# Performance work log

Measured on AMD Instinct MI355X. Metric: run time of the kernel, lower is better.

## Reference

```python
import jax, jax.numpy as jnp
import numpy as np

TOPK_POS = 16
TOPK_NEG = 16
EPS = 1e-12  # F.normalize default eps


def _l2norm(x):
    # torch.nn.functional.normalize(p=2, dim=1): x / max(||x||_2, eps)
    n = jnp.sqrt(jnp.sum(x * x, axis=1, keepdims=True))
    return x / jnp.maximum(n, EPS)


def setup_inputs() -> dict:
    key = jax.random.key(0)
    k0, k1, k2, k3, k4 = jax.random.split(key, 5)
    B, I, J, C = 32, 1024, 2048, 1024
    f_rad = jax.random.normal(k0, (B, I), dtype=jnp.float32)
    f_histo = jax.random.normal(k1, (B, J), dtype=jnp.float32)
    rad_mask = jax.random.randint(k2, (B,), 0, 2).astype(bool)
    histo_mask = jax.random.randint(k3, (B,), 0, 2).astype(bool)
    # nn.Linear(in_channels*2, out_channels): weight [C, 2*I], bias [C]
    W = jax.random.normal(k4, (C, 2 * I), dtype=jnp.float32) / np.sqrt(2 * I)
    b = jnp.zeros((C,), dtype=jnp.float32)
    token = jnp.zeros((1, C), dtype=jnp.float32)  # missing_modality_token
    return {"f_rad": f_rad, "f_histo": f_histo, "rad_mask": rad_mask,
            "histo_mask": histo_mask, "W": W, "b": b, "token": token}


def reference(f_rad, f_histo, rad_mask, histo_mask, W, b, token):
    r = _l2norm(f_rad)            # [B, I]
    h = _l2norm(f_histo)          # [B, J]
    sim = jnp.einsum('bi,bj->bij', r, h)  # [B, I, J]
    pos_map = jnp.mean(jax.lax.top_k(sim, TOPK_POS)[0], axis=-1)    # [B, I]
    neg_map = jnp.mean(jax.lax.top_k(-sim, TOPK_NEG)[0], axis=-1)   # [B, I]
    # cat([B,1,I],[B,1,I], dim=1).view(B,-1) == concat(pos, neg) along features
    feat = jnp.concatenate([pos_map, neg_map], axis=1)  # [B, 2I]
    emb = feat @ W.T + b                                 # [B, C]
    # modality_flags = ~torch.min(rad_mask, histo_mask)  (bool AND then NOT)
    flags = (~(rad_mask & histo_mask)).astype(emb.dtype)[:, None]  # [B, 1]
    return emb + token * flags
```

## Files before the change

kernel.cpp:

```cpp
#include <hip/hip_runtime.h>
#include <math.h>

#define NB 32
#define NI 1024
#define NJ 2048
#define NC 1024
#define K2 2048

__device__ __forceinline__ void merge16(float* __restrict__ v,
                                        const float* __restrict__ w) {
    float m[16];
#pragma unroll
    for (int i = 0; i < 16; ++i) m[i] = fmaxf(v[i], w[15 - i]);
#pragma unroll
    for (int st = 8; st >= 1; st >>= 1)
#pragma unroll
        for (int i = 0; i < 16; ++i)
            if ((i & st) == 0) {
                float x = m[i], y = m[i + st];
                m[i] = fmaxf(x, y);
                m[i + st] = fminf(x, y);
            }
#pragma unroll
    for (int i = 0; i < 16; ++i) v[i] = m[i];
}

__global__ __launch_bounds__(256)
void prep_kernel(const float* __restrict__ f_rad,
                 const float* __restrict__ f_histo,
                 const unsigned char* __restrict__ rad_mask,
                 const unsigned char* __restrict__ histo_mask,
                 const float* __restrict__ bias,
                 const float* __restrict__ token,
                 float* __restrict__ F,
                 float* __restrict__ out)
{
    __shared__ float listsP[256][16];
    __shared__ float listsN[256][16];
    __shared__ float red[4];

    const int b = blockIdx.x;
    const int t = threadIdx.x;
    const int wave = t >> 6, lane = t & 63;

    float hv[8];
    float ss = 0.f;
#pragma unroll
    for (int i = 0; i < 8; ++i) {
        hv[i] = f_histo[b * NJ + t + i * 256];
        ss += hv[i] * hv[i];
    }
#pragma unroll
    for (int off = 1; off < 64; off <<= 1) ss += __shfl_xor(ss, off, 64);
    if (lane == 0) red[wave] = ss;

    float vp[16], vn[16];
#pragma unroll
    for (int i = 0; i < 8; ++i) { vp[i] = hv[i]; vn[i] = -hv[i]; }
#pragma unroll
    for (int i = 8; i < 16; ++i) { vp[i] = -INFINITY; vn[i] = -INFINITY; }
#pragma unroll
    for (int a = 0; a < 7; ++a)
#pragma unroll
        for (int c = 0; c < 7 - a; ++c) {
            float x = vp[c], y = vp[c + 1];
            vp[c] = fmaxf(x, y); vp[c + 1] = fminf(x, y);
            x = vn[c]; y = vn[c + 1];
            vn[c] = fmaxf(x, y); vn[c + 1] = fminf(x, y);
        }

    __syncthreads();
    const float hnorm = fmaxf(sqrtf(red[0] + red[1] + red[2] + red[3]), 1e-12f);

#pragma unroll
    for (int i = 0; i < 16; ++i) { listsP[t][i] = vp[i]; listsN[t][i] = vn[i]; }
    __syncthreads();

#pragma unroll
    for (int s = 128; s >= 1; s >>= 1) {
        if (t < s) {
            float wp[16], wn[16];
#pragma unroll
            for (int i = 0; i < 16; ++i) { wp[i] = listsP[t + s][i]; wn[i] = listsN[t + s][i]; }
            merge16(vp, wp);
            merge16(vn, wn);
#pragma unroll
            for (int i = 0; i < 16; ++i) { listsP[t][i] = vp[i]; listsN[t][i] = vn[i]; }
        }
        __syncthreads();
    }

    float sumP = 0.f, sumN = 0.f;
#pragma unroll
    for (int i = 0; i < 16; ++i) { sumP += listsP[0][i]; sumN += listsN[0][i]; }
    const float Hpos = sumP / (16.f * hnorm);
    const float Hneg = -sumN / (16.f * hnorm);

    float rv[4];
    float ss2 = 0.f;
#pragma unroll
    for (int i = 0; i < 4; ++i) {
        rv[i] = f_rad[b * NI + t + i * 256];
        ss2 += rv[i] * rv[i];
    }
#pragma unroll
    for (int off = 1; off < 64; off <<= 1) ss2 += __shfl_xor(ss2, off, 64);
    __syncthreads();
    if (lane == 0) red[wave] = ss2;
    __syncthreads();
    const float rnorm = fmaxf(sqrtf(red[0] + red[1] + red[2] + red[3]), 1e-12f);

#pragma unroll
    for (int i = 0; i < 4; ++i) {
        float rn = rv[i] / rnorm;
        float p, q;
        if (rn > 0.f) { p = rn * Hpos;  q = -rn * Hneg; }
        else          { p = rn * Hneg;  q = -rn * Hpos; }
        F[b * K2 + t + i * 256]      = p;
        F[b * K2 + NI + t + i * 256] = q;
    }

    const float flag = (rad_mask[b] != 0 && histo_mask[b] != 0) ? 0.f : 1.f;
#pragma unroll
    for (int i = 0; i < NC / 256; ++i) {
        int c = t + i * 256;
        out[b * NC + c] = bias[c] + token[c] * flag;
    }
}

__global__ __launch_bounds__(256, 4)
void gemm_kernel(const float4* __restrict__ F4,
                 const float4* __restrict__ WF4,
                 float* __restrict__ out)
{
    const int t = threadIdx.x;
    const int wave = t >> 6, lane = t & 63;
    const int c0 = blockIdx.x * 8 + wave * 2;
    const int kk4 = blockIdx.y * 64 + lane;

    const float4 w0 = WF4[(size_t)c0 * 512 + kk4];
    const float4 w1 = WF4[(size_t)(c0 + 1) * 512 + kk4];

    float acc0[32], acc1[32];
#pragma unroll
    for (int b = 0; b < 32; ++b) { acc0[b] = 0.f; acc1[b] = 0.f; }

#pragma unroll
    for (int bb = 0; bb < 32; bb += 4) {
        float4 fv[4];
#pragma unroll
        for (int u = 0; u < 4; ++u) fv[u] = F4[(bb + u) * 512 + kk4];
#pragma unroll
        for (int u = 0; u < 4; ++u) {
            const int b = bb + u;
            acc0[b] = fmaf(fv[u].x, w0.x, acc0[b]);
            acc0[b] = fmaf(fv[u].y, w0.y, acc0[b]);
            acc0[b] = fmaf(fv[u].z, w0.z, acc0[b]);
            acc0[b] = fmaf(fv[u].w, w0.w, acc0[b]);
            acc1[b] = fmaf(fv[u].x, w1.x, acc1[b]);
            acc1[b] = fmaf(fv[u].y, w1.y, acc1[b]);
            acc1[b] = fmaf(fv[u].z, w1.z, acc1[b]);
            acc1[b] = fmaf(fv[u].w, w1.w, acc1[b]);
        }
    }

    const bool odd = lane & 1;
    float z[32];
#pragma unroll
    for (int b = 0; b < 32; ++b) {
        float send = odd ? acc0[b] : acc1[b];
        float recv = __shfl_xor(send, 1, 64);
        z[b] = (odd ? acc1[b] : acc0[b]) + recv;
    }

#pragma unroll
    for (int j = 0; j < 5; ++j) {
        const int o = 2 << j;
        const bool hi = (lane & o) != 0;
        const int n = 32 >> (j + 1);
#pragma unroll
        for (int m = 0; m < n; ++m) {
            float send = hi ? z[2 * m] : z[2 * m + 1];
            float recv = __shfl_xor(send, o, 64);
            z[m] = (hi ? z[2 * m + 1] : z[2 * m]) + recv;
        }
    }

    atomicAdd(&out[(lane >> 1) * NC + c0 + (lane & 1)], z[0]);
}

extern "C" void kernel_launch(void* const* d_in, const int* in_sizes, int n_in,
                              void* d_out, int out_size, void* d_ws, size_t ws_size,
                              hipStream_t stream) {
    const float* f_rad       = (const float*)d_in[0];
    const float* f_histo     = (const float*)d_in[1];
    const unsigned char* rm  = (const unsigned char*)d_in[2];
    const unsigned char* hm  = (const unsigned char*)d_in[3];
    const float* W           = (const float*)d_in[4];
    const float* bias        = (const float*)d_in[5];
    const float* token       = (const float*)d_in[6];
    float* out = (float*)d_out;
    float* F   = (float*)d_ws;

    prep_kernel<<<NB, 256, 0, stream>>>(f_rad, f_histo, rm, hm, bias, token, F, out);
    dim3 grid(128, 8);
    gemm_kernel<<<grid, 256, 0, stream>>>((const float4*)F, (const float4*)W, out);
}
```

Before: 90.74 us.

## Replace shared-memory top-k tree reduction with wave shuffle merges and vectorize prep loads

The prep kernel's 8-level shared-memory tree reduction of per-thread top-16 lists, which needed a block barrier at every level, is replaced by intra-wave shuffle-based bitonic merges, followed by a small final merge of four per-wave lists in shared memory. All global loads and stores in prep (histo, rad, bias, token, F, out) become float4 accesses, and the rad norm reduction is computed alongside the histo norm to drop extra barriers. The aim is to cut the serialized reduction latency of the 32-block prep kernel. In exchange it does many register shuffles, and every thread redundantly performs the final 4-way merge.

```diff
diff --git a/kernel.cpp b/kernel.cpp
--- a/kernel.cpp
+++ b/kernel.cpp
@@ -25,107 +25,149 @@
     for (int i = 0; i < 16; ++i) v[i] = m[i];
 }
 
+__device__ __forceinline__ void merge8to16(const float* __restrict__ a,
+                                           const float* __restrict__ w,
+                                           float* __restrict__ m) {
+#pragma unroll
+    for (int i = 0; i < 8; ++i) m[i] = a[i];
+#pragma unroll
+    for (int i = 0; i < 8; ++i) m[8 + i] = w[7 - i];
+#pragma unroll
+    for (int st = 8; st >= 1; st >>= 1)
+#pragma unroll
+        for (int i = 0; i < 16; ++i)
+            if ((i & st) == 0) {
+                float x = m[i], y = m[i + st];
+                m[i] = fmaxf(x, y);
+                m[i + st] = fminf(x, y);
+            }
+}
+
+__device__ __forceinline__ void sort8_desc(float* __restrict__ v) {
+#pragma unroll
+    for (int a = 0; a < 7; ++a)
+#pragma unroll
+        for (int c = 0; c < 7 - a; ++c) {
+            float x = v[c], y = v[c + 1];
+            v[c] = fmaxf(x, y);
+            v[c + 1] = fminf(x, y);
+        }
+}
+
 __global__ __launch_bounds__(256)
-void prep_kernel(const float* __restrict__ f_rad,
-                 const float* __restrict__ f_histo,
+void prep_kernel(const float4* __restrict__ R4,
+                 const float4* __restrict__ H4,
                  const unsigned char* __restrict__ rad_mask,
                  const unsigned char* __restrict__ histo_mask,
-                 const float* __restrict__ bias,
-                 const float* __restrict__ token,
-                 float* __restrict__ F,
-                 float* __restrict__ out)
+                 const float4* __restrict__ bias4,
+                 const float4* __restrict__ token4,
+                 float4* __restrict__ F4,
+                 float4* __restrict__ out4)
 {
-    __shared__ float listsP[256][16];
-    __shared__ float listsN[256][16];
-    __shared__ float red[4];
+    __shared__ __align__(16) float wlP[4][16];
+    __shared__ __align__(16) float wlN[4][16];
+    __shared__ float redH[4], redR[4];
 
     const int b = blockIdx.x;
     const int t = threadIdx.x;
     const int wave = t >> 6, lane = t & 63;
 
-    float hv[8];
-    float ss = 0.f;
-#pragma unroll
-    for (int i = 0; i < 8; ++i) {
-        hv[i] = f_histo[b * NJ + t + i * 256];
-        ss += hv[i] * hv[i];
-    }
+    const float4 h0 = H4[b * 512 + t];
+    const float4 h1 = H4[b * 512 + 256 + t];
+    const float4 rv4 = R4[b * 256 + t];
+    const float4 bv = bias4[t];
+    const float4 tv = token4[t];
+
+    float ss = h0.x * h0.x + h0.y * h0.y + h0.z * h0.z + h0.w * h0.w
+             + h1.x * h1.x + h1.y * h1.y + h1.z * h1.z + h1.w * h1.w;
 #pragma unroll
     for (int off = 1; off < 64; off <<= 1) ss += __shfl_xor(ss, off, 64);
-    if (lane == 0) red[wave] = ss;
+    if (lane == 0) redH[wave] = ss;
+
+    float ss2 = rv4.x * rv4.x + rv4.y * rv4.y + rv4.z * rv4.z + rv4.w * rv4.w;
+#pragma unroll
+    for (int off = 1; off < 64; off <<= 1) ss2 += __shfl_xor(ss2, off, 64);
+    if (lane == 0) redR[wave] = ss2;
+
+    float sp[8] = {h0.x, h0.y, h0.z, h0.w, h1.x, h1.y, h1.z, h1.w};
+    float sn[8];
+#pragma unroll
+    for (int i = 0; i < 8; ++i) sn[i] = -sp[i];
+    sort8_desc(sp);
+    sort8_desc(sn);
 
     float vp[16], vn[16];
-#pragma unroll
-    for (int i = 0; i < 8; ++i) { vp[i] = hv[i]; vn[i] = -hv[i]; }
-#pragma unroll
-    for (int i = 8; i < 16; ++i) { vp[i] = -INFINITY; vn[i] = -INFINITY; }
-#pragma unroll
-    for (int a = 0; a < 7; ++a)
-#pragma unroll
-        for (int c = 0; c < 7 - a; ++c) {
-            float x = vp[c], y = vp[c + 1];
-            vp[c] = fmaxf(x, y); vp[c + 1] = fminf(x, y);
-            x = vn[c]; y = vn[c + 1];
-            vn[c] = fmaxf(x, y); vn[c + 1] = fminf(x, y);
-        }
-
+    {
+        float wp8[8], wn8[8];
+#pragma unroll
+        for (int i = 0; i < 8; ++i) {
+            wp8[i] = __shfl_xor(sp[i], 1, 64);
+            wn8[i] = __shfl_xor(sn[i], 1, 64);
+        }
+        merge8to16(sp, wp8, vp);
+        merge8to16(sn, wn8, vn);
+    }
+#pragma unroll
+    for (int off = 2; off <= 32; off <<= 1) {
+        float wp[16], wn[16];
+#pragma unroll
+        for (int i = 0; i < 16; ++i) {
+            wp[i] = __shfl_xor(vp[i], off, 64);
+            wn[i] = __shfl_xor(vn[i], off, 64);
+        }
+        merge16(vp, wp);
+        merge16(vn, wn);
+    }
+
+    if (lane == 0) {
+#pragma unroll
+        for (int i = 0; i < 16; ++i) { wlP[wave][i] = vp[i]; wlN[wave][i] = vn[i]; }
+    }
     __syncthreads();
-    const float hnorm = fmaxf(sqrtf(red[0] + red[1] + red[2] + red[3]), 1e-12f);
-
-#pragma unroll
-    for (int i = 0; i < 16; ++i) { listsP[t][i] = vp[i]; listsN[t][i] = vn[i]; }
-    __syncthreads();
-
-#pragma unroll
-    for (int s = 128; s >= 1; s >>= 1) {
-        if (t < s) {
-            float wp[16], wn[16];
-#pragma unroll
-            for (int i = 0; i < 16; ++i) { wp[i] = listsP[t + s][i]; wn[i] = listsN[t + s][i]; }
-            merge16(vp, wp);
-            merge16(vn, wn);
-#pragma unroll
-            for (int i = 0; i < 16; ++i) { listsP[t][i] = vp[i]; listsN[t][i] = vn[i]; }
-        }
-        __syncthreads();
-    }
+
+    float aP[16], bP[16], cP[16], dP[16];
+#pragma unroll
+    for (int i = 0; i < 16; ++i) {
+        aP[i] = wlP[0][i]; bP[i] = wlP[1][i];
+        cP[i] = wlP[2][i]; dP[i] = wlP[3][i];
+    }
+    merge16(aP, bP); merge16(cP, dP); merge16(aP, cP);
+    float aN[16], bN[16], cN[16], dN[16];
+#pragma unroll
+    for (int i = 0; i < 16; ++i) {
+        aN[i] = wlN[0][i]; bN[i] = wlN[1][i];
+        cN[i] = wlN[2][i]; dN[i] = wlN[3][i];
+    }
+    merge16(aN, bN); merge16(cN, dN); merge16(aN, cN);
 
     float sumP = 0.f, sumN = 0.f;
 #pragma unroll
-    for (int i = 0; i < 16; ++i) { sumP += listsP[0][i]; sumN += listsN[0][i]; }
+    for (int i = 0; i < 16; ++i) { sumP += aP[i]; sumN += aN[i]; }
+
+    const float hnorm = fmaxf(sqrtf(redH[0] + redH[1] + redH[2] + redH[3]), 1e-12f);
+    const float rnorm = fmaxf(sqrtf(redR[0] + redR[1] + redR[2] + redR[3]), 1e-12f);
     const float Hpos = sumP / (16.f * hnorm);
     const float Hneg = -sumN / (16.f * hnorm);
-
-    float rv[4];
-    float ss2 = 0.f;
-#pragma unroll
-    for (int i = 0; i < 4; ++i) {
-        rv[i] = f_rad[b * NI + t + i * 256];
-        ss2 += rv[i] * rv[i];
-    }
-#pragma unroll
-    for (int off = 1; off < 64; off <<= 1) ss2 += __shfl_xor(ss2, off, 64);
-    __syncthreads();
-    if (lane == 0) red[wave] = ss2;
-    __syncthreads();
-    const float rnorm = fmaxf(sqrtf(red[0] + red[1] + red[2] + red[3]), 1e-12f);
-
-#pragma unroll
-    for (int i = 0; i < 4; ++i) {
-        float rn = rv[i] / rnorm;
-        float p, q;
-        if (rn > 0.f) { p = rn * Hpos;  q = -rn * Hneg; }
-        else          { p = rn * Hneg;  q = -rn * Hpos; }
-        F[b * K2 + t + i * 256]      = p;
-        F[b * K2 + NI + t + i * 256] = q;
-    }
+    const float inv_r = 1.f / rnorm;
+
+    float4 p, q;
+    {
+        float rn;
+        rn = rv4.x * inv_r; p.x = rn * (rn > 0.f ? Hpos : Hneg); q.x = -rn * (rn > 0.f ? Hneg : Hpos);
+        rn = rv4.y * inv_r; p.y = rn * (rn > 0.f ? Hpos : Hneg); q.y = -rn * (rn > 0.f ? Hneg : Hpos);
+        rn = rv4.z * inv_r; p.z = rn * (rn > 0.f ? Hpos : Hneg); q.z = -rn * (rn > 0.f ? Hneg : Hpos);
+        rn = rv4.w * inv_r; p.w = rn * (rn > 0.f ? Hpos : Hneg); q.w = -rn * (rn > 0.f ? Hneg : Hpos);
+    }
+    F4[b * 512 + t] = p;
+    F4[b * 512 + 256 + t] = q;
 
     const float flag = (rad_mask[b] != 0 && histo_mask[b] != 0) ? 0.f : 1.f;
-#pragma unroll
-    for (int i = 0; i < NC / 256; ++i) {
-        int c = t + i * 256;
-        out[b * NC + c] = bias[c] + token[c] * flag;
-    }
+    float4 o;
+    o.x = bv.x + tv.x * flag;
+    o.y = bv.y + tv.y * flag;
+    o.z = bv.z + tv.z * flag;
+    o.w = bv.w + tv.w * flag;
+    out4[b * 256 + t] = o;
 }
 
 __global__ __launch_bounds__(256, 4)
@@ -202,7 +244,10 @@
     float* out = (float*)d_out;
     float* F   = (float*)d_ws;
 
-    prep_kernel<<<NB, 256, 0, stream>>>(f_rad, f_histo, rm, hm, bias, token, F, out);
+    prep_kernel<<<NB, 256, 0, stream>>>((const float4*)f_rad, (const float4*)f_histo,
+                                        rm, hm, (const float4*)bias,
+                                        (const float4*)token,
+                                        (float4*)F, (float4*)out);
     dim3 grid(128, 8);
     gemm_kernel<<<grid, 256, 0, stream>>>((const float4*)F, (const float4*)W, out);
 }
```

Result: faster. 88.85 us (-2.1%).
